# Performance work log

Measured on AMD Instinct MI355X. Metric: run time of the kernel, lower is better.

The kernel has to match this reference:

```python
import jax, jax.numpy as jnp
import numpy as np

S, B, D, W = 2048, 4, 1024, 256  # seq_len, batch, d_model, local_window_size


def create_local_mask(seq_len, w):
    # Faithful to source: tril(w-1) then tril(-(w-1)) -> keeps j <= i-(w-1)
    m = jnp.ones((seq_len, seq_len), dtype=bool)
    m = jnp.tril(m, w - 1)
    m = jnp.tril(m, -(w - 1))
    return m


def setup_inputs() -> dict:
    key = jax.random.key(0)
    ks = jax.random.split(key, 12)
    w = lambda k: jax.random.normal(k, (D, D), dtype=jnp.float32) * 0.02
    return {
        "query": jax.random.normal(ks[0], (S, B, D), dtype=jnp.float32),
        "key_in": jax.random.normal(ks[1], (S, B, D), dtype=jnp.float32),
        "value": jax.random.normal(ks[2], (S, B, D), dtype=jnp.float32),
        "Wq": w(ks[3]), "bq": jnp.zeros((D,), jnp.float32),
        "Wk": w(ks[4]), "bk": jnp.zeros((D,), jnp.float32),
        "Wv": w(ks[5]), "bv": jnp.zeros((D,), jnp.float32),
        "pos_bias": jax.random.normal(ks[6], (S, S), dtype=jnp.float32) * 0.02,
        "Wo": w(ks[7]), "bo": jnp.zeros((D,), jnp.float32),
        "mask": jnp.ones((S, S, 1), dtype=bool),
    }


def reference(query, key_in, value, Wq, bq, Wk, bk, Wv, bv, pos_bias, Wo, bo, mask):
    # Linear projections (torch Linear: x @ W.T + b)
    q = jnp.einsum('sbd,ed->sbe', query, Wq) + bq
    k = jnp.einsum('sbd,ed->sbe', key_in, Wk) + bk
    v = jnp.einsum('sbd,ed->sbe', value, Wv) + bv

    local_mask = create_local_mask(S, W)
    pb = (pos_bias * local_mask.astype(pos_bias.dtype))[:, :, None]  # [S,S,1]
    pb = jnp.where(mask, pb, -jnp.inf)

    max_key = jnp.max(k, axis=0, keepdims=True)          # [1,B,D]
    max_pb = jnp.max(pb, axis=1, keepdims=True)          # [S,1,1]
    exp_key = jnp.exp(k - max_key)                       # [S,B,D]
    exp_pb = jnp.exp(pb - max_pb)                        # [S,S,B] after broadcast

    num = jnp.einsum('ijb,jbd->ibd', exp_pb, exp_key * v)
    den = jnp.einsum('ijb,jbd->ibd', exp_pb, exp_key)
    y = jax.nn.sigmoid(q) * num / den
    return jnp.einsum('sbd,ed->sbe', y, Wo) + bo
```

## Files before the change

kernel.cpp:

```cpp
#include <hip/hip_runtime.h>
#include <hip/hip_bf16.h>
#include <cstdint>


typedef short short8 __attribute__((ext_vector_type(8)));
typedef float f32x4 __attribute__((ext_vector_type(4)));

#define S_LEN 2048
#define NBD 4096
#define SBD 8388608
#define DD 1048576
#define SS 4194304

#define ASZ 8192
#define BUFSZ 24576
#define GASZ 4096
#define GBUF 12288
#define OASZ 2048
#define OBUF 10240
#define AS1 __attribute__((address_space(1)))
#define AS3 __attribute__((address_space(3)))

__device__ __forceinline__ unsigned short f2bf(float f) {
  union { float f; unsigned int u; } x; x.f = f;
  unsigned int u = x.u;
  unsigned int r = u + 0x7fffu + ((u >> 16) & 1u);
  return (unsigned short)(r >> 16);
}
__device__ __forceinline__ float bf2f(unsigned short b) {
  union { unsigned int u; float f; } x; x.u = ((unsigned int)b) << 16;
  return x.f;
}

__global__ __launch_bounds__(256) void k_cvt3(
    const float* __restrict__ a, const float* __restrict__ b, const float* __restrict__ c,
    unsigned short* __restrict__ oa, unsigned short* __restrict__ ob,
    unsigned short* __restrict__ oc) {
  const int w = blockIdx.x;
  const int arr = w >> 11;
  const int b2 = w & 2047;
  const float* src = arr == 0 ? a : (arr == 1 ? b : c);
  unsigned short* dst = arr == 0 ? oa : (arr == 1 ? ob : oc);
  const size_t t0 = (size_t)b2 * 256 + threadIdx.x;
#pragma unroll
  for (int it = 0; it < 2; ++it) {
    const size_t base = (t0 + (size_t)it * 524288) * 8;
    float4 x0 = *(const float4*)(src + base);
    float4 x1 = *(const float4*)(src + base + 4);
    short8 s;
    s[0] = (short)f2bf(x0.x); s[1] = (short)f2bf(x0.y);
    s[2] = (short)f2bf(x0.z); s[3] = (short)f2bf(x0.w);
    s[4] = (short)f2bf(x1.x); s[5] = (short)f2bf(x1.y);
    s[6] = (short)f2bf(x1.z); s[7] = (short)f2bf(x1.w);
    *(short8*)(dst + base) = s;
  }
}

__global__ void k_cvt4w(const float* __restrict__ wq, const float* __restrict__ wk,
                        const float* __restrict__ wv, const float* __restrict__ wo,
                        unsigned short* __restrict__ wcat, unsigned short* __restrict__ wob) {
  int i = (blockIdx.x * blockDim.x + threadIdx.x) * 4;
  float4 fq = *(const float4*)(wq + i);
  float4 fk = *(const float4*)(wk + i);
  float4 fv = *(const float4*)(wv + i);
  float4 fo = *(const float4*)(wo + i);
  ushort4 u;
  u.x = f2bf(fq.x); u.y = f2bf(fq.y); u.z = f2bf(fq.z); u.w = f2bf(fq.w);
  *(ushort4*)(wcat + i) = u;
  u.x = f2bf(fk.x); u.y = f2bf(fk.y); u.z = f2bf(fk.z); u.w = f2bf(fk.w);
  *(ushort4*)(wcat + DD + i) = u;
  u.x = f2bf(fv.x); u.y = f2bf(fv.y); u.z = f2bf(fv.z); u.w = f2bf(fv.w);
  *(ushort4*)(wcat + 2 * DD + i) = u;
  u.x = f2bf(fo.x); u.y = f2bf(fo.y); u.z = f2bf(fo.z); u.w = f2bf(fo.w);
  *(ushort4*)(wob + i) = u;
}

__global__ void k_build_c(const float* __restrict__ pb, unsigned short* __restrict__ C) {
  int i4 = (blockIdx.x * blockDim.x + threadIdx.x) * 4;
  float4 p = *(const float4*)(pb + i4);
  const int i = i4 >> 11;
  const int j = i4 & 2047;
  ushort4 o;
  o.x = f2bf((i >= j + 255) ? expm1f(p.x) : 0.0f);
  o.y = f2bf((i >= j + 256) ? expm1f(p.y) : 0.0f);
  o.z = f2bf((i >= j + 257) ? expm1f(p.z) : 0.0f);
  o.w = f2bf((i >= j + 258) ? expm1f(p.w) : 0.0f);
  *(ushort4*)(C + i4) = o;
}

__global__ __launch_bounds__(256) void k_eu_transpose(
    const unsigned short* __restrict__ kbf, const unsigned short* __restrict__ vbf,
    unsigned short* __restrict__ Mt, float* __restrict__ totals) {
  __shared__ unsigned short Lu[64][65];
  __shared__ unsigned short Le[64][65];
  const int n0 = blockIdx.x * 64;
  const int j0 = blockIdx.y * 64;
  const int t = threadIdx.x;
  const int c = t & 63;
  const int jq = t >> 6;
  float ptu = 0.f, pte = 0.f;
#pragma unroll 4
  for (int s = 0; s < 16; ++s) {
    int jj = jq + s * 4;
    size_t g = (size_t)(j0 + jj) * NBD + n0 + c;
    float kv = bf2f(kbf[g]);
    float vv = bf2f(vbf[g]);
    float e = __expf(kv);
    float u = e * vv;
    Le[jj][c] = f2bf(e);
    Lu[jj][c] = f2bf(u);
    pte += e; ptu += u;
  }
  atomicAdd(&totals[n0 + c], ptu);
  atomicAdd(&totals[NBD + n0 + c], pte);
  __syncthreads();
  const int jj2 = t & 63;
  const int nq = t >> 6;
#pragma unroll 4
  for (int s = 0; s < 16; ++s) {
    int nn = nq + s * 4;
    int ru = 2 * n0 + 32 * (nn >> 4) + (nn & 15);
    Mt[(size_t)ru * S_LEN + j0 + jj2] = Lu[jj2][nn];
    Mt[(size_t)(ru + 16) * S_LEN + j0 + jj2] = Le[jj2][nn];
  }
}

#define SBAR() do { __builtin_amdgcn_sched_barrier(0); __builtin_amdgcn_s_barrier(); \
                    __builtin_amdgcn_sched_barrier(0); } while (0)
#define VM(n)  do { asm volatile("s_waitcnt vmcnt(" #n ")" ::: "memory"); \
                    __builtin_amdgcn_sched_barrier(0); } while (0)
#define LGK0() do { asm volatile("s_waitcnt lgkmcnt(0)" ::: "memory"); \
                    __builtin_amdgcn_sched_barrier(0); } while (0)

#define G32_STAGE(tile, bidx) do {                                                        \
    const int k0_ = (tile) * 32;                                                          \
    __builtin_amdgcn_global_load_lds(                                                     \
        (const AS1 unsigned int*)(Ag + (size_t)(m0 + wave * 16 + lr4) * 1024 + k0_ + lc4),\
        (AS3 unsigned int*)&lds[(bidx) * GBUF + wave * 512 + lane * 8], 16, 0, 0);        \
    _Pragma("unroll") for (int q_ = 0; q_ < 2; ++q_) {                                    \
      const int g_ = wave * 2 + q_;                                                       \
      __builtin_amdgcn_global_load_lds(                                                   \
          (const AS1 unsigned int*)(Bg + (size_t)(n0 + g_ * 16 + lr4) * 1024 + k0_ + lc4),\
          (AS3 unsigned int*)&lds[(bidx) * GBUF + GASZ + g_ * 512 + lane * 8], 16, 0, 0); \
    }                                                                                     \
  } while (0)

#define G32_READF(RA, RB, bidx) do {                                                      \
    _Pragma("unroll") for (int f_ = 0; f_ < 4; ++f_)                                      \
      RA[f_] = *(const short8*)&lds[(bidx) * GBUF + (wr + f_ * 16 + l15) * 32 + swg];     \
    _Pragma("unroll") for (int f_ = 0; f_ < 4; ++f_)                                      \
      RB[f_] = *(const short8*)&lds[(bidx) * GBUF + GASZ + (wc + f_ * 16 + l15) * 32 + swg];\
  } while (0)

#define G32_MFMA(RA, RB) do {                                                             \
    __builtin_amdgcn_s_setprio(1);                                                        \
    _Pragma("unroll") for (int i_ = 0; i_ < 4; ++i_)                                      \
    _Pragma("unroll") for (int j_ = 0; j_ < 4; ++j_)                                      \
      acc[i_][j_] = __builtin_amdgcn_mfma_f32_16x16x32_bf16(RA[i_], RB[j_],               \
                                                            acc[i_][j_], 0, 0, 0);       \
    __builtin_amdgcn_s_setprio(0);                                                        \
  } while (0)

__global__ __launch_bounds__(512, 4) void k_qkv32(
    const unsigned short* __restrict__ A0, const unsigned short* __restrict__ A1,
    const unsigned short* __restrict__ A2, const unsigned short* __restrict__ Bg,
    const float* __restrict__ b0, const float* __restrict__ b1, const float* __restrict__ b2,
    unsigned short* __restrict__ o0, unsigned short* __restrict__ o1,
    unsigned short* __restrict__ o2) {
  __shared__ unsigned short lds[3 * GBUF];

  const int tid = threadIdx.x;
  const int wave = tid >> 6, lane = tid & 63;
  const int l15 = lane & 15, lh = lane >> 4;
  const int swg = (lh ^ ((l15 >> 1) & 3)) * 8;
  const int lr4 = lane >> 2;
  const int lc4 = ((lane & 3) ^ ((lane >> 3) & 3)) * 8;
  const int wr = (wave >> 2) * 64, wc = (wave & 3) * 64;

  const int w = blockIdx.x;
  const int xcd = w & 7, slot = w >> 3;
  const int mb = xcd * 8 + slot / 12;
  const int nb = slot % 12;
  const int m0 = mb * 128, n0 = nb * 256;
  const int grp = nb >> 2;
  const unsigned short* Ag = grp == 0 ? A0 : (grp == 1 ? A1 : A2);

  f32x4 acc[4][4];
#pragma unroll
  for (int i = 0; i < 4; ++i)
#pragma unroll
    for (int j = 0; j < 4; ++j)
      acc[i][j] = (f32x4){0.f, 0.f, 0.f, 0.f};

  short8 ra[4], rb[4];
  const int NT = 32;

  G32_STAGE(0, 0);
  G32_STAGE(1, 1);
  G32_STAGE(2, 2);
  VM(6);
  SBAR();
  G32_READF(ra, rb, 0);
  int cb = 0;
  for (int t = 0; t < NT; ++t) {
    G32_MFMA(ra, rb);
    if (t == NT - 1) break;
    LGK0();
    if (t + 2 <= NT - 1) VM(3); else VM(0);
    SBAR();
    int nbuf = cb + 1; if (nbuf == 3) nbuf = 0;
    G32_READF(ra, rb, nbuf);
    if (t + 3 <= NT - 1) G32_STAGE(t + 3, cb);
    cb = nbuf;
  }

  const float* bias = grp == 0 ? b0 : (grp == 1 ? b1 : b2);
  unsigned short* outp = grp == 0 ? o0 : (grp == 1 ? o1 : o2);
#pragma unroll
  for (int i = 0; i < 4; ++i)
#pragma unroll
    for (int j = 0; j < 4; ++j)
#pragma unroll
      for (int r = 0; r < 4; ++r) {
        const int row = m0 + wr + i * 16 + lh * 4 + r;
        const int col = (n0 + wc + j * 16 + l15) & 1023;
        float v = acc[i][j][r] + bias[col];
        if (grp == 0) v = 1.0f / (1.0f + __expf(-v));
        outp[(size_t)row * 1024 + col] = f2bf(v);
      }
}

#define O32_STAGE(tile, bidx) do {                                                        \
    const int k0_ = (tile) * 32;                                                          \
    __builtin_amdgcn_global_load_lds(                                                     \
        (const AS1 unsigned int*)(Ag + (size_t)(m0 + aseg * 16 + lr4) * 1024 + k0_ + lc4),\
        (AS3 unsigned int*)&lds[(bidx) * OBUF + aseg * 512 + lane * 8], 16, 0, 0);        \
    _Pragma("unroll") for (int q_ = 0; q_ < 2; ++q_) {                                    \
      const int g_ = wave * 2 + q_;                                                       \
      __builtin_amdgcn_global_load_lds(                                                   \
          (const AS1 unsigned int*)(Bg + (size_t)(n0 + g_ * 16 + lr4) * 1024 + k0_ + lc4),\
          (AS3 unsigned int*)&lds[(bidx) * OBUF + OASZ + g_ * 512 + lane * 8], 16, 0, 0); \
    }                                                                                     \
  } while (0)

#define O32_READF(RA, RB, bidx) do {                                                      \
    _Pragma("unroll") for (int f_ = 0; f_ < 2; ++f_)                                      \
      RA[f_] = *(const short8*)&lds[(bidx) * OBUF + (wr + f_ * 16 + l15) * 32 + swg];     \
    _Pragma("unroll") for (int f_ = 0; f_ < 4; ++f_)                                      \
      RB[f_] = *(const short8*)&lds[(bidx) * OBUF + OASZ + (wc + f_ * 16 + l15) * 32 + swg];\
  } while (0)

#define O32_MFMA(RA, RB) do {                                                             \
    __builtin_amdgcn_s_setprio(1);                                                        \
    _Pragma("unroll") for (int i_ = 0; i_ < 2; ++i_)                                      \
    _Pragma("unroll") for (int j_ = 0; j_ < 4; ++j_)                                      \
      acc[i_][j_] = __builtin_amdgcn_mfma_f32_16x16x32_bf16(RA[i_], RB[j_],               \
                                                            acc[i_][j_], 0, 0, 0);       \
    __builtin_amdgcn_s_setprio(0);                                                        \
  } while (0)

__global__ __launch_bounds__(512, 4) void k_out64(
    const unsigned short* __restrict__ Ag, const unsigned short* __restrict__ Bg,
    const float* __restrict__ bias, float* __restrict__ outp) {
  __shared__ unsigned short lds[3 * OBUF];

  const int tid = threadIdx.x;
  const int wave = tid >> 6, lane = tid & 63;
  const int l15 = lane & 15, lh = lane >> 4;
  const int swg = (lh ^ ((l15 >> 1) & 3)) * 8;
  const int lr4 = lane >> 2;
  const int lc4 = ((lane & 3) ^ ((lane >> 3) & 3)) * 8;
  const int aseg = wave & 3;
  const int wr = (wave >> 2) * 32, wc = (wave & 3) * 64;

  const int w = blockIdx.x;
  const int xcd = w & 7, slot = w >> 3;
  const int mb = xcd * 16 + (slot >> 2);
  const int nb = slot & 3;
  const int m0 = mb * 64, n0 = nb * 256;

  f32x4 acc[2][4];
#pragma unroll
  for (int i = 0; i < 2; ++i)
#pragma unroll
    for (int j = 0; j < 4; ++j)
      acc[i][j] = (f32x4){0.f, 0.f, 0.f, 0.f};

  short8 ra[2], rb[4];
  const int NT = 32;

  O32_STAGE(0, 0);
  O32_STAGE(1, 1);
  O32_STAGE(2, 2);
  VM(6);
  SBAR();
  O32_READF(ra, rb, 0);
  int cb = 0;
  for (int t = 0; t < NT; ++t) {
    O32_MFMA(ra, rb);
    if (t == NT - 1) break;
    LGK0();
    if (t + 2 <= NT - 1) VM(3); else VM(0);
    SBAR();
    int nbuf = cb + 1; if (nbuf == 3) nbuf = 0;
    O32_READF(ra, rb, nbuf);
    if (t + 3 <= NT - 1) O32_STAGE(t + 3, cb);
    cb = nbuf;
  }

#pragma unroll
  for (int i = 0; i < 2; ++i)
#pragma unroll
    for (int j = 0; j < 4; ++j)
#pragma unroll
      for (int r = 0; r < 4; ++r) {
        const int row = m0 + wr + i * 16 + lh * 4 + r;
        const int col = n0 + wc + j * 16 + l15;
        outp[(size_t)row * 1024 + col] = acc[i][j][r] + bias[col];
      }
}

#define STAGE(tile, bidx) do {                                                            \
    const int k0s_ = (tile) * 64;                                                         \
    _Pragma("unroll") for (int q_ = 0; q_ < 2; ++q_) {                                    \
      const int g_ = wave * 2 + q_;                                                       \
      __builtin_amdgcn_global_load_lds(                                                   \
          (const AS1 unsigned int*)(Ag + (size_t)(m0 + g_ * 8 + lr) * 2048 + k0s_ + lc),  \
          (AS3 unsigned int*)&lds[(bidx) * BUFSZ + g_ * 512], 16, 0, 0);                  \
    }                                                                                     \
    _Pragma("unroll") for (int q_ = 0; q_ < 4; ++q_) {                                    \
      const int g_ = wave * 4 + q_;                                                       \
      __builtin_amdgcn_global_load_lds(                                                   \
          (const AS1 unsigned int*)(Bg + (size_t)(n0 + g_ * 8 + lr) * 2048 + k0s_ + lc),  \
          (AS3 unsigned int*)&lds[(bidx) * BUFSZ + ASZ + g_ * 512], 16, 0, 0);            \
    }                                                                                     \
  } while (0)

#define READF(RA, RB, bidx, ks) do {                                                      \
    const int kof_ = (ks) * 32 + lh8;                                                     \
    _Pragma("unroll") for (int f_ = 0; f_ < 4; ++f_) {                                    \
      const int row_ = wr + f_ * 16 + l15;                                                \
      RA[f_] = *(const short8*)&lds[(bidx) * BUFSZ + row_ * 64 + (kof_ ^ swz)];           \
    }                                                                                     \
    _Pragma("unroll") for (int f_ = 0; f_ < 4; ++f_) {                                    \
      const int row_ = wc + f_ * 16 + l15;                                                \
      RB[f_] = *(const short8*)&lds[(bidx) * BUFSZ + ASZ + row_ * 64 + (kof_ ^ swz)];     \
    }                                                                                     \
  } while (0)

#define MFMA16(RA, RB) do {                                                               \
    __builtin_amdgcn_s_setprio(1);                                                        \
    _Pragma("unroll") for (int i_ = 0; i_ < 4; ++i_)                                      \
    _Pragma("unroll") for (int j_ = 0; j_ < 4; ++j_)                                      \
      acc[i_][j_] = __builtin_amdgcn_mfma_f32_16x16x32_bf16(RA[i_], RB[j_],               \
                                                            acc[i_][j_], 0, 0, 0);       \
    __builtin_amdgcn_s_setprio(0);                                                        \
  } while (0)

__global__ __launch_bounds__(512, 2) void k_tri(
    const unsigned short* __restrict__ Ag, const unsigned short* __restrict__ Bg,
    const float* __restrict__ totals, const unsigned short* __restrict__ sq,
    unsigned short* __restrict__ Y) {
  __shared__ unsigned short lds[3 * BUFSZ];

  const int tid = threadIdx.x;
  const int wave = tid >> 6, lane = tid & 63;
  const int l15 = lane & 15, lh = lane >> 4;
  const int lh8 = lh * 8;
  const int swz = (l15 & 7) * 8;
  const int lr = lane >> 3;
  const int lc = ((lane & 7) ^ lr) * 8;
  const int wr = (wave >> 2) * 64, wc = (wave & 3) * 64;

  const int w = blockIdx.x;
  const int mb = 15 - (w >> 5);
  const int nb = w & 31;
  const int m0 = mb * 128, n0 = nb * 256;
  const int NT = mb > 0 ? 2 * mb - 1 : 0;

  f32x4 acc[4][4];
#pragma unroll
  for (int i = 0; i < 4; ++i)
#pragma unroll
    for (int j = 0; j < 4; ++j)
      acc[i][j] = (f32x4){0.f, 0.f, 0.f, 0.f};

  short8 ra0[4], rb0[4], ra1[4], rb1[4];

  if (NT > 0) {
    STAGE(0, 0);
    if (NT > 1) STAGE(1, 1);
    if (NT > 2) STAGE(2, 2);
    if (NT > 2) VM(12); else if (NT > 1) VM(6); else VM(0);
    SBAR();
    READF(ra0, rb0, 0, 0);
    int cb = 0;
    for (int t = 0; t < NT; ++t) {
      READF(ra1, rb1, cb, 1);
      MFMA16(ra0, rb0);
      if (t < NT - 1) {
        LGK0();
        if (t + 2 <= NT - 1) VM(6); else VM(0);
        SBAR();
        int nbuf = cb + 1; if (nbuf == 3) nbuf = 0;
        READF(ra0, rb0, nbuf, 0);
        if (t + 3 <= NT - 1) STAGE(t + 3, cb);
        cb = nbuf;
        MFMA16(ra1, rb1);
      } else {
        MFMA16(ra1, rb1);
      }
    }
  }

#pragma unroll
  for (int i = 0; i < 4; ++i)
#pragma unroll
    for (int p = 0; p < 2; ++p) {
      const int n = ((n0 + wc) >> 1) + 16 * p + l15;
      const float tu = totals[n];
      const float te = totals[NBD + n];
#pragma unroll
      for (int r = 0; r < 4; ++r) {
        const int row = m0 + wr + i * 16 + lh * 4 + r;
        const size_t idx = (size_t)row * NBD + n;
        const float num = tu + acc[i][2 * p][r];
        const float den = te + acc[i][2 * p + 1][r];
        Y[idx] = f2bf(bf2f(sq[idx]) * num / den);
      }
    }
}

extern "C" void kernel_launch(void* const* d_in, const int* in_sizes, int n_in,
                              void* d_out, int out_size, void* d_ws, size_t ws_size,
                              hipStream_t stream) {
  const float* query   = (const float*)d_in[0];
  const float* key_in  = (const float*)d_in[1];
  const float* value   = (const float*)d_in[2];
  const float* Wq      = (const float*)d_in[3];
  const float* bq      = (const float*)d_in[4];
  const float* Wk      = (const float*)d_in[5];
  const float* bk      = (const float*)d_in[6];
  const float* Wv      = (const float*)d_in[7];
  const float* bv      = (const float*)d_in[8];
  const float* pos_bias= (const float*)d_in[9];
  const float* Wo      = (const float*)d_in[10];
  const float* bo      = (const float*)d_in[11];
  float* out = (float*)d_out;

  char* wp = (char*)d_ws;
  auto alloc = [&](size_t bytes) -> char* {
    char* p = wp;
    wp += (bytes + 255) & ~(size_t)255;
    return p;
  };
  unsigned short* Xq   = (unsigned short*)alloc((size_t)SBD * 2);
  unsigned short* Xk   = (unsigned short*)alloc((size_t)SBD * 2);
  unsigned short* Xv   = (unsigned short*)alloc((size_t)SBD * 2);
  unsigned short* Wcat = (unsigned short*)alloc((size_t)3 * DD * 2);
  unsigned short* Wob  = (unsigned short*)alloc((size_t)DD * 2);
  unsigned short* Cb   = (unsigned short*)alloc((size_t)SS * 2);
  unsigned short* sigq = (unsigned short*)alloc((size_t)SBD * 2);
  unsigned short* kbf  = (unsigned short*)alloc((size_t)SBD * 2);
  unsigned short* vbf  = (unsigned short*)alloc((size_t)SBD * 2);
  unsigned short* Mt   = (unsigned short*)alloc((size_t)8192 * S_LEN * 2);
  float*          tot  = (float*)alloc((size_t)8192 * 4);
  unsigned short* Yb   = (unsigned short*)alloc((size_t)SBD * 2);

  k_cvt3<<<6144, 256, 0, stream>>>(query, key_in, value, Xq, Xk, Xv);
  k_cvt4w<<<DD / 4 / 256, 256, 0, stream>>>(Wq, Wk, Wv, Wo, Wcat, Wob);

  k_build_c<<<SS / 4 / 256, 256, 0, stream>>>(pos_bias, Cb);

  k_qkv32<<<768, 512, 0, stream>>>(Xq, Xk, Xv, Wcat, bq, bk, bv, sigq, kbf, vbf);

  hipMemsetAsync(tot, 0, 8192 * sizeof(float), stream);
  dim3 ge(NBD / 64, S_LEN / 64);
  k_eu_transpose<<<ge, 256, 0, stream>>>(kbf, vbf, Mt, tot);

  k_tri<<<512, 512, 0, stream>>>(Cb, Mt, tot, sigq, Yb);

  k_out64<<<512, 512, 0, stream>>>(Yb, Wob, bo, out);
}
```

Measured before the change: 183.2 us.

## Replace output projection GEMM with 128x256 tile, K=64 double-fragment pipeline

Swaps the 64x256-tile, K=32-step output GEMM for a 128x256-tile kernel that stages 64-wide K slices and reuses the READF/MFMA16 macros from the k_tri kernel. Each wave interleaves two half-K fragment reads with MFMAs, and the grid drops from 512 to 256 blocks. The aim is higher arithmetic intensity per LDS load and fewer barriers per unit of K. In exchange it uses more LDS and registers (occupancy 2 instead of 4) and launches fewer blocks, which on a 256-CU part gives exactly one block per CU.

```diff
diff --git a/kernel.cpp b/kernel.cpp
--- a/kernel.cpp
+++ b/kernel.cpp
@@ -16,8 +16,6 @@
 #define BUFSZ 24576
 #define GASZ 4096
 #define GBUF 12288
-#define OASZ 2048
-#define OBUF 10240
 #define AS1 __attribute__((address_space(1)))
 #define AS3 __attribute__((address_space(3)))
 
@@ -227,96 +225,6 @@
         float v = acc[i][j][r] + bias[col];
         if (grp == 0) v = 1.0f / (1.0f + __expf(-v));
         outp[(size_t)row * 1024 + col] = f2bf(v);
-      }
-}
-
-#define O32_STAGE(tile, bidx) do {                                                        \
-    const int k0_ = (tile) * 32;                                                          \
-    __builtin_amdgcn_global_load_lds(                                                     \
-        (const AS1 unsigned int*)(Ag + (size_t)(m0 + aseg * 16 + lr4) * 1024 + k0_ + lc4),\
-        (AS3 unsigned int*)&lds[(bidx) * OBUF + aseg * 512 + lane * 8], 16, 0, 0);        \
-    _Pragma("unroll") for (int q_ = 0; q_ < 2; ++q_) {                                    \
-      const int g_ = wave * 2 + q_;                                                       \
-      __builtin_amdgcn_global_load_lds(                                                   \
-          (const AS1 unsigned int*)(Bg + (size_t)(n0 + g_ * 16 + lr4) * 1024 + k0_ + lc4),\
-          (AS3 unsigned int*)&lds[(bidx) * OBUF + OASZ + g_ * 512 + lane * 8], 16, 0, 0); \
-    }                                                                                     \
-  } while (0)
-
-#define O32_READF(RA, RB, bidx) do {                                                      \
-    _Pragma("unroll") for (int f_ = 0; f_ < 2; ++f_)                                      \
-      RA[f_] = *(const short8*)&lds[(bidx) * OBUF + (wr + f_ * 16 + l15) * 32 + swg];     \
-    _Pragma("unroll") for (int f_ = 0; f_ < 4; ++f_)                                      \
-      RB[f_] = *(const short8*)&lds[(bidx) * OBUF + OASZ + (wc + f_ * 16 + l15) * 32 + swg];\
-  } while (0)
-
-#define O32_MFMA(RA, RB) do {                                                             \
-    __builtin_amdgcn_s_setprio(1);                                                        \
-    _Pragma("unroll") for (int i_ = 0; i_ < 2; ++i_)                                      \
-    _Pragma("unroll") for (int j_ = 0; j_ < 4; ++j_)                                      \
-      acc[i_][j_] = __builtin_amdgcn_mfma_f32_16x16x32_bf16(RA[i_], RB[j_],               \
-                                                            acc[i_][j_], 0, 0, 0);       \
-    __builtin_amdgcn_s_setprio(0);                                                        \
-  } while (0)
-
-__global__ __launch_bounds__(512, 4) void k_out64(
-    const unsigned short* __restrict__ Ag, const unsigned short* __restrict__ Bg,
-    const float* __restrict__ bias, float* __restrict__ outp) {
-  __shared__ unsigned short lds[3 * OBUF];
-
-  const int tid = threadIdx.x;
-  const int wave = tid >> 6, lane = tid & 63;
-  const int l15 = lane & 15, lh = lane >> 4;
-  const int swg = (lh ^ ((l15 >> 1) & 3)) * 8;
-  const int lr4 = lane >> 2;
-  const int lc4 = ((lane & 3) ^ ((lane >> 3) & 3)) * 8;
-  const int aseg = wave & 3;
-  const int wr = (wave >> 2) * 32, wc = (wave & 3) * 64;
-
-  const int w = blockIdx.x;
-  const int xcd = w & 7, slot = w >> 3;
-  const int mb = xcd * 16 + (slot >> 2);
-  const int nb = slot & 3;
-  const int m0 = mb * 64, n0 = nb * 256;
-
-  f32x4 acc[2][4];
-#pragma unroll
-  for (int i = 0; i < 2; ++i)
-#pragma unroll
-    for (int j = 0; j < 4; ++j)
-      acc[i][j] = (f32x4){0.f, 0.f, 0.f, 0.f};
-
-  short8 ra[2], rb[4];
-  const int NT = 32;
-
-  O32_STAGE(0, 0);
-  O32_STAGE(1, 1);
-  O32_STAGE(2, 2);
-  VM(6);
-  SBAR();
-  O32_READF(ra, rb, 0);
-  int cb = 0;
-  for (int t = 0; t < NT; ++t) {
-    O32_MFMA(ra, rb);
-    if (t == NT - 1) break;
-    LGK0();
-    if (t + 2 <= NT - 1) VM(3); else VM(0);
-    SBAR();
-    int nbuf = cb + 1; if (nbuf == 3) nbuf = 0;
-    O32_READF(ra, rb, nbuf);
-    if (t + 3 <= NT - 1) O32_STAGE(t + 3, cb);
-    cb = nbuf;
-  }
-
-#pragma unroll
-  for (int i = 0; i < 2; ++i)
-#pragma unroll
-    for (int j = 0; j < 4; ++j)
-#pragma unroll
-      for (int r = 0; r < 4; ++r) {
-        const int row = m0 + wr + i * 16 + lh * 4 + r;
-        const int col = n0 + wc + j * 16 + l15;
-        outp[(size_t)row * 1024 + col] = acc[i][j][r] + bias[col];
       }
 }
 
@@ -431,6 +339,83 @@
     }
 }
 
+#define OSTAGE(tile, bidx) do {                                                           \
+    const int k0s_ = (tile) * 64;                                                         \
+    _Pragma("unroll") for (int q_ = 0; q_ < 2; ++q_) {                                    \
+      const int g_ = wave * 2 + q_;                                                       \
+      __builtin_amdgcn_global_load_lds(                                                   \
+          (const AS1 unsigned int*)(Ag + (size_t)(m0 + g_ * 8 + lr) * 1024 + k0s_ + lc),  \
+          (AS3 unsigned int*)&lds[(bidx) * BUFSZ + g_ * 512], 16, 0, 0);                  \
+    }                                                                                     \
+    _Pragma("unroll") for (int q_ = 0; q_ < 4; ++q_) {                                    \
+      const int g_ = wave * 4 + q_;                                                       \
+      __builtin_amdgcn_global_load_lds(                                                   \
+          (const AS1 unsigned int*)(Bg + (size_t)(n0 + g_ * 8 + lr) * 1024 + k0s_ + lc),  \
+          (AS3 unsigned int*)&lds[(bidx) * BUFSZ + ASZ + g_ * 512], 16, 0, 0);            \
+    }                                                                                     \
+  } while (0)
+
+__global__ __launch_bounds__(512, 2) void k_gout(
+    const unsigned short* __restrict__ Ag, const unsigned short* __restrict__ Bg,
+    const float* __restrict__ bias, float* __restrict__ outp) {
+  __shared__ unsigned short lds[3 * BUFSZ];
+
+  const int tid = threadIdx.x;
+  const int wave = tid >> 6, lane = tid & 63;
+  const int l15 = lane & 15, lh = lane >> 4;
+  const int lh8 = lh * 8;
+  const int swz = (l15 & 7) * 8;
+  const int lr = lane >> 3;
+  const int lc = ((lane & 7) ^ lr) * 8;
+  const int wr = (wave >> 2) * 64, wc = (wave & 3) * 64;
+
+  const int w = blockIdx.x;
+  const int xcd = w & 7, slot = w >> 3;
+  const int mb = xcd * 8 + (slot >> 2), nb = slot & 3;
+  const int m0 = mb * 128, n0 = nb * 256;
+
+  f32x4 acc[4][4];
+#pragma unroll
+  for (int i = 0; i < 4; ++i)
+#pragma unroll
+    for (int j = 0; j < 4; ++j)
+      acc[i][j] = (f32x4){0.f, 0.f, 0.f, 0.f};
+
+  short8 ra0[4], rb0[4], ra1[4], rb1[4];
+
+  OSTAGE(0, 0); OSTAGE(1, 1); OSTAGE(2, 2);
+  VM(12);
+  SBAR();
+  READF(ra0, rb0, 0, 0);
+  int cb = 0;
+  const int NT = 16;
+  for (int t = 0; t < NT; ++t) {
+    READF(ra1, rb1, cb, 1);
+    MFMA16(ra0, rb0);
+    if (t < NT - 1) {
+      LGK0();
+      if (t + 2 <= NT - 1) VM(6); else VM(0);
+      SBAR();
+      int nbuf = cb + 1; if (nbuf == 3) nbuf = 0;
+      READF(ra0, rb0, nbuf, 0);
+      if (t + 3 <= NT - 1) OSTAGE(t + 3, cb);
+      cb = nbuf;
+    }
+    MFMA16(ra1, rb1);
+  }
+
+#pragma unroll
+  for (int i = 0; i < 4; ++i)
+#pragma unroll
+    for (int j = 0; j < 4; ++j)
+#pragma unroll
+      for (int r = 0; r < 4; ++r) {
+        const int row = m0 + wr + i * 16 + lh * 4 + r;
+        const int col = n0 + wc + j * 16 + l15;
+        outp[(size_t)row * 1024 + col] = acc[i][j][r] + bias[col];
+      }
+}
+
 extern "C" void kernel_launch(void* const* d_in, const int* in_sizes, int n_in,
                               void* d_out, int out_size, void* d_ws, size_t ws_size,
                               hipStream_t stream) {
@@ -480,5 +465,5 @@
 
   k_tri<<<512, 512, 0, stream>>>(Cb, Mt, tot, sigq, Yb);
 
-  k_out64<<<512, 512, 0, stream>>>(Yb, Wob, bo, out);
-}
+  k_gout<<<256, 512, 0, stream>>>(Yb, Wob, bo, out);
+}
```

Result: no change. 181.9 us (-0.7%).
